# Kernel optimization log

Hardware: AMD Instinct MI355X
Metric: run time of the kernel (lower is better)

## Reference

```python
import jax, jax.numpy as jnp
import numpy as np

V, B, P = 32, 128, 256   # views/directions, batch, max points per diagram
J = 75                   # n_elements (structure elements)
NF = 32                  # n_filters (= directions)
S2 = 25                  # stage_2_out
NU = 0.1
BN_EPS = 1e-5


def _transform(births, lifetimes):
    """UpperDiagonalThresholdedLogTransform(nu=0.1) on (birth, death) points."""
    deaths = births + lifetimes + 0.01
    inv = jnp.asarray(1.0 / np.sqrt(2.0), births.dtype)
    x = (births + deaths) * inv          # rotated 1st coord
    y = (deaths - births) * inv          # rotated 2nd coord (persistence), > 0
    y = jnp.where(y <= NU, jnp.log(y / NU) * NU + NU, y)
    return jnp.stack([x, y], axis=-1)    # [V,B,P,2]


def _batchnorm(x, gamma, beta, axis):
    mean = x.mean(axis=axis, keepdims=True)
    var = x.var(axis=axis, keepdims=True)  # biased, training-mode BN
    return (x - mean) / jnp.sqrt(var + BN_EPS) * gamma + beta


def setup_inputs() -> dict:
    key = jax.random.key(0)
    ks = jax.random.split(key, 20)
    inp = {
        "births": jax.random.uniform(ks[0], (V, B, P), jnp.float32),
        "lifetimes": jax.random.uniform(ks[1], (V, B, P), jnp.float32),
        "mask": jax.random.randint(ks[2], (V, B, P), 0, 2).astype(jnp.int32),
        # SLayerPHT params (one SLayer per view)
        "centers": jax.random.uniform(ks[3], (V, J, 2), jnp.float32),
        "sharpness": 4.0 + 0.1 * jax.random.normal(ks[4], (V, J, 2), jnp.float32),
        # stage_1: Conv1d(3->NF, k=1, no bias), Conv1d(NF->8, k=1, no bias)
        "w1": 0.1 * jax.random.normal(ks[5], (V, NF, 3), jnp.float32),
        "w2": 0.1 * jax.random.normal(ks[6], (V, 8, NF), jnp.float32),
        # stage_2: Linear(J->S2), BN(S2), Linear(S2->S2)
        "l1_w": 0.1 * jax.random.normal(ks[7], (V, S2, J), jnp.float32),
        "l1_b": 0.1 * jax.random.normal(ks[8], (V, S2), jnp.float32),
        "bn1_g": jnp.ones((V, S2), jnp.float32),
        "bn1_b": jnp.zeros((V, S2), jnp.float32),
        "l2_w": 0.1 * jax.random.normal(ks[9], (V, S2, S2), jnp.float32),
        "l2_b": 0.1 * jax.random.normal(ks[10], (V, S2), jnp.float32),
        # linear_1: Linear(V*S2 -> 500) + BN(500); linear_2: Linear(500 -> 200)
        "fc1_w": 0.05 * jax.random.normal(ks[11], (500, V * S2), jnp.float32),
        "fc1_b": 0.05 * jax.random.normal(ks[12], (500,), jnp.float32),
        "bn2_g": jnp.ones((500,), jnp.float32),
        "bn2_b": jnp.zeros((500,), jnp.float32),
        "fc2_w": 0.05 * jax.random.normal(ks[13], (200, 500), jnp.float32),
        "fc2_b": 0.05 * jax.random.normal(ks[14], (200,), jnp.float32),
    }
    return inp


def reference(births, lifetimes, mask, centers, sharpness, w1, w2,
              l1_w, l1_b, bn1_g, bn1_b, l2_w, l2_b,
              fc1_w, fc1_b, bn2_g, bn2_b, fc2_w, fc2_b):
    q = _transform(births, lifetimes)                 # [V,B,P,2]
    m = mask.astype(q.dtype)                          # [V,B,P]
    # SLayer: z[v,b,j] = sum_p m * exp(-sum_d s[v,j,d]^2 (q[v,b,p,d]-c[v,j,d])^2)
    s2 = sharpness * sharpness                        # [V,J,2]
    qa = jnp.concatenate([q * q, q, jnp.ones_like(q[..., :1])], axis=-1)  # [V,B,P,5]
    ca = jnp.concatenate([s2, -2.0 * s2 * centers,
                          (s2 * centers * centers).sum(-1, keepdims=True)], axis=-1)  # [V,J,5]
    d2 = jnp.einsum('vbpk,vjk->vbpj', qa, ca)         # squared weighted distance
    z = jnp.einsum('vbpj,vbp->vbj', jnp.exp(-d2), m)  # [V,B,J]
    # neighbor-direction stacking (n_neighbor_directions=1, cyclic): [i-1, i, i+1]
    zn = jnp.stack([jnp.roll(z, 1, axis=0), z, jnp.roll(z, -1, axis=0)], axis=2)  # [V,B,3,J]
    # stage_1: two 1x1 conv1d (no bias), then max over channels
    h = jnp.einsum('vbcj,vfc->vbfj', zn, w1)          # [V,B,NF,J]
    h = jnp.einsum('vbfj,vgf->vbgj', h, w2)           # [V,B,8,J]
    h = h.max(axis=2)                                 # [V,B,J]
    # stage_2: Linear -> BN(train) -> Linear -> ReLU (Dropout = eval identity)
    u = jnp.einsum('vbj,voj->vbo', h, l1_w) + l1_b[:, None, :]   # [V,B,S2]
    u = _batchnorm(u, bn1_g[:, None, :], bn1_b[:, None, :], axis=1)
    u = jnp.einsum('vbo,vpo->vbp', u, l2_w) + l2_b[:, None, :]
    u = jax.nn.relu(u)
    x = u.transpose(1, 0, 2).reshape(B, V * S2)       # torch.cat(x, 1)
    x = x @ fc1_w.T + fc1_b
    x = _batchnorm(x, bn2_g, bn2_b, axis=0)
    x = x @ fc2_w.T + fc2_b                           # [B,200]
    return x
```

## Files before the change

kernel.cpp:

```cpp
#include <hip/hip_runtime.h>

#define V 32
#define B 128
#define P 256
#define J 75
#define NF 32
#define S2 25

__global__ __launch_bounds__(128) void slayer_kernel(
    const float* __restrict__ births,
    const float* __restrict__ lifetimes,
    const int* __restrict__ mask,
    const float* __restrict__ centers,
    const float* __restrict__ sharpness,
    float* __restrict__ z)
{
    const int vb = blockIdx.x;
    const int v  = vb >> 7;
    const int tid = threadIdx.x;
    const int lane = tid & 63;

    __shared__ float4 pts[P];
    __shared__ int cnt;

    if (tid == 0) cnt = 0;
    __syncthreads();

    const float inv = 0.70710678118654752f;
    #pragma unroll
    for (int c = 0; c < 2; ++c) {
        const int p  = tid + c * 128;
        const int gi = vb * P + p;
        float b0 = births[gi];
        float l0 = lifetimes[gi];
        int   m  = mask[gi];
        float d  = b0 + l0 + 0.01f;
        float x  = (b0 + d) * inv;
        float y  = (d - b0) * inv;
        if (y <= 0.1f) y = __logf(y * 10.0f) * 0.1f + 0.1f;

        bool keep = (m != 0);
        unsigned long long bal = __ballot(keep);
        unsigned long long lt  = (1ull << lane) - 1ull;
        int prefix = __popcll(bal & lt);
        int total  = __popcll(bal);
        int base = 0;
        if (lane == 0) base = atomicAdd(&cnt, total);
        base = __shfl(base, 0, 64);
        if (keep) pts[base + prefix] = make_float4(x, y, x * x, y * y);
    }
    __syncthreads();

    const int n = cnt;
    if (tid < J) {
        const int cj = (v * J + tid) * 2;
        float cx = centers[cj + 0];
        float cy = centers[cj + 1];
        float sx = sharpness[cj + 0];
        float sy = sharpness[cj + 1];
        float s2x = sx * sx, s2y = sy * sy;
        float k0 = -s2x;
        float k1 = -s2y;
        float k2 = 2.0f * s2x * cx;
        float k3 = 2.0f * s2y * cy;
        float kc = -(s2x * cx * cx + s2y * cy * cy);
        float acc = 0.f;
        #pragma unroll 4
        for (int p = 0; p < n; ++p) {
            float4 a = pts[p];
            float d = fmaf(k0, a.z, kc);
            d = fmaf(k1, a.w, d);
            d = fmaf(k2, a.x, d);
            d = fmaf(k3, a.y, d);
            acc += __expf(d);
        }
        z[vb * J + tid] = acc;
    }
}

__global__ __launch_bounds__(128) void stage12_kernel(
    const float* __restrict__ z,
    const float* __restrict__ w1,
    const float* __restrict__ w2,
    const float* __restrict__ l1_w,
    const float* __restrict__ l1_b,
    float* __restrict__ u_pre)
{
    const int vb = blockIdx.x;
    const int v  = vb >> 7;
    const int b  = vb & 127;
    const int vm = (v + V - 1) & (V - 1);
    const int vp = (v + 1) & (V - 1);
    const int tid = threadIdx.x;

    __shared__ float z0[J], z1[J], z2[J];
    __shared__ float w1s[NF * 3];
    __shared__ float w2s[8 * NF];
    __shared__ float hsh[J];

    if (tid < J) {
        z0[tid] = z[(vm * B + b) * J + tid];
        z1[tid] = z[(v  * B + b) * J + tid];
        z2[tid] = z[(vp * B + b) * J + tid];
    }
    if (tid < NF * 3) w1s[tid] = w1[v * NF * 3 + tid];
    w2s[tid]       = w2[v * 8 * NF + tid];
    w2s[tid + 128] = w2[v * 8 * NF + tid + 128];
    __syncthreads();

    if (tid < J) {
        float a0 = z0[tid], a1 = z1[tid], a2 = z2[tid];
        float hf[NF];
        #pragma unroll
        for (int f = 0; f < NF; ++f)
            hf[f] = w1s[f * 3 + 0] * a0 + w1s[f * 3 + 1] * a1 + w1s[f * 3 + 2] * a2;
        float hm = -3.4e38f;
        #pragma unroll
        for (int g = 0; g < 8; ++g) {
            float s = 0.f;
            #pragma unroll
            for (int f = 0; f < NF; ++f) s += w2s[g * NF + f] * hf[f];
            hm = fmaxf(hm, s);
        }
        hsh[tid] = hm;
    }
    __syncthreads();

    if (tid < S2) {
        float acc = l1_b[v * S2 + tid];
        const float* wrow = l1_w + (v * S2 + tid) * J;
        for (int j = 0; j < J; ++j) acc += hsh[j] * wrow[j];
        u_pre[vb * S2 + tid] = acc;
    }
}

__global__ __launch_bounds__(256) void bn1_l2_kernel(
    const float* __restrict__ u_pre,
    const float* __restrict__ bn1_g,
    const float* __restrict__ bn1_b,
    const float* __restrict__ l2_w,
    const float* __restrict__ l2_b,
    float* __restrict__ xT)
{
    const int v = blockIdx.x;
    const int tid = threadIdx.x;

    __shared__ float u[B * S2];
    __shared__ float w[S2 * S2];
    __shared__ float sc[S2], sh[S2];

    for (int i = tid; i < B * S2; i += 256) u[i] = u_pre[v * B * S2 + i];
    for (int i = tid; i < S2 * S2; i += 256) w[i] = l2_w[v * S2 * S2 + i];
    __syncthreads();

    if (tid < S2) {
        float s = 0.f, ss = 0.f;
        for (int b = 0; b < B; ++b) {
            float x = u[b * S2 + tid];
            s += x; ss += x * x;
        }
        float mean = s * (1.f / B);
        float var  = ss * (1.f / B) - mean * mean;
        float istd = rsqrtf(var + 1e-5f);
        float g  = bn1_g[v * S2 + tid];
        float be = bn1_b[v * S2 + tid];
        sc[tid] = g * istd;
        sh[tid] = be - mean * g * istd;
    }
    __syncthreads();

    for (int i = tid; i < B * S2; i += 256) {
        int o = i % S2;
        u[i] = u[i] * sc[o] + sh[o];
    }
    __syncthreads();

    for (int i = tid; i < B * S2; i += 256) {
        int b = i & 127;
        int p = i >> 7;
        float acc = l2_b[v * S2 + p];
        #pragma unroll
        for (int o = 0; o < S2; ++o) acc += u[b * S2 + o] * w[p * S2 + o];
        acc = fmaxf(acc, 0.f);
        xT[(v * S2 + p) * B + b] = acc;
    }
}

#define FC1_TILE 2
__global__ __launch_bounds__(128) void fc1_bn2_kernel(
    const float* __restrict__ xT,
    const float* __restrict__ fc1_w,
    const float* __restrict__ fc1_b,
    const float* __restrict__ bn2_g,
    const float* __restrict__ bn2_b,
    float* __restrict__ y1n)
{
    const int n0 = blockIdx.x * FC1_TILE;
    const int tid = threadIdx.x;
    const int K = V * S2;

    __shared__ float wsm[FC1_TILE][V * S2];
    __shared__ float red[2][2][FC1_TILE];

    for (int i = tid; i < FC1_TILE * K; i += 128) {
        int ni = i / K;
        int k  = i - ni * K;
        wsm[ni][k] = fc1_w[(n0 + ni) * K + k];
    }
    __syncthreads();

    float acc[FC1_TILE] = {0.f, 0.f};
    for (int k = 0; k < K; ++k) {
        float xv = xT[k * B + tid];
        #pragma unroll
        for (int ni = 0; ni < FC1_TILE; ++ni) acc[ni] += xv * wsm[ni][k];
    }

    const int wave = tid >> 6;
    const int lane = tid & 63;
    #pragma unroll
    for (int ni = 0; ni < FC1_TILE; ++ni) {
        acc[ni] += fc1_b[n0 + ni];
        float s = acc[ni], ss = acc[ni] * acc[ni];
        #pragma unroll
        for (int off = 32; off > 0; off >>= 1) {
            s  += __shfl_down(s,  off, 64);
            ss += __shfl_down(ss, off, 64);
        }
        if (lane == 0) { red[wave][0][ni] = s; red[wave][1][ni] = ss; }
    }
    __syncthreads();

    #pragma unroll
    for (int ni = 0; ni < FC1_TILE; ++ni) {
        float s  = red[0][0][ni] + red[1][0][ni];
        float ss = red[0][1][ni] + red[1][1][ni];
        float mean = s * (1.f / B);
        float var  = ss * (1.f / B) - mean * mean;
        float istd = rsqrtf(var + 1e-5f);
        float g  = bn2_g[n0 + ni];
        float be = bn2_b[n0 + ni];
        float scl = g * istd;
        y1n[(n0 + ni) * B + tid] = acc[ni] * scl + (be - mean * scl);
    }
}

__global__ __launch_bounds__(128) void fc2_kernel(
    const float* __restrict__ y1n,
    const float* __restrict__ fc2_w,
    const float* __restrict__ fc2_b,
    float* __restrict__ out)
{
    const int k = blockIdx.x;
    const int tid = threadIdx.x;

    __shared__ float wsm[500];
    for (int i = tid; i < 500; i += 128) wsm[i] = fc2_w[k * 500 + i];
    __syncthreads();

    float acc = fc2_b[k];
    for (int n = 0; n < 500; ++n) acc += y1n[n * B + tid] * wsm[n];
    out[tid * 200 + k] = acc;
}

extern "C" void kernel_launch(void* const* d_in, const int* in_sizes, int n_in,
                              void* d_out, int out_size, void* d_ws, size_t ws_size,
                              hipStream_t stream) {
    const float* births    = (const float*)d_in[0];
    const float* lifetimes = (const float*)d_in[1];
    const int*   mask      = (const int*)d_in[2];
    const float* centers   = (const float*)d_in[3];
    const float* sharpness = (const float*)d_in[4];
    const float* w1        = (const float*)d_in[5];
    const float* w2        = (const float*)d_in[6];
    const float* l1_w      = (const float*)d_in[7];
    const float* l1_b      = (const float*)d_in[8];
    const float* bn1_g     = (const float*)d_in[9];
    const float* bn1_b     = (const float*)d_in[10];
    const float* l2_w      = (const float*)d_in[11];
    const float* l2_b      = (const float*)d_in[12];
    const float* fc1_w     = (const float*)d_in[13];
    const float* fc1_b     = (const float*)d_in[14];
    const float* bn2_g     = (const float*)d_in[15];
    const float* bn2_b     = (const float*)d_in[16];
    const float* fc2_w     = (const float*)d_in[17];
    const float* fc2_b     = (const float*)d_in[18];
    float* out = (float*)d_out;

    float* ws    = (float*)d_ws;
    float* z     = ws;
    float* u_pre = ws + 307200;
    float* xT    = ws + 307200 + 102400;
    float* y1n   = ws + 307200 + 102400 + 102400;

    slayer_kernel <<<V * B, 128, 0, stream>>>(births, lifetimes, mask, centers, sharpness, z);
    stage12_kernel<<<V * B, 128, 0, stream>>>(z, w1, w2, l1_w, l1_b, u_pre);
    bn1_l2_kernel <<<V, 256, 0, stream>>>(u_pre, bn1_g, bn1_b, l2_w, l2_b, xT);
    fc1_bn2_kernel<<<(500 / FC1_TILE), 128, 0, stream>>>(xT, fc1_w, fc1_b, bn2_g, bn2_b, y1n);
    fc2_kernel    <<<200, 128, 0, stream>>>(y1n, fc2_w, fc2_b, out);
}
```

Before: 184.0 us.

## Split reductions across more threads in all kernels and batch stage12 per block

The SLayer kernel now uses 256 threads and splits the point loop three ways per center, combining the partial sums through shared memory. stage12 handles three batch rows per block, caches l1_w in shared memory and spreads the l1 dot products over more threads. The BN1 statistics, fc1 and fc2 split their K reductions across extra threads. The aim is to fix low thread utilisation, where only 75 or 25 threads were active, at the cost of extra syncs and shared-memory traffic.

```diff
diff --git a/kernel.cpp b/kernel.cpp
--- a/kernel.cpp
+++ b/kernel.cpp
@@ -7,7 +7,7 @@
 #define NF 32
 #define S2 25
 
-__global__ __launch_bounds__(128) void slayer_kernel(
+__global__ __launch_bounds__(256) void slayer_kernel(
     const float* __restrict__ births,
     const float* __restrict__ lifetimes,
     const int* __restrict__ mask,
@@ -22,15 +22,14 @@
 
     __shared__ float4 pts[P];
     __shared__ int cnt;
+    __shared__ float part[2][J];
 
     if (tid == 0) cnt = 0;
     __syncthreads();
 
     const float inv = 0.70710678118654752f;
-    #pragma unroll
-    for (int c = 0; c < 2; ++c) {
-        const int p  = tid + c * 128;
-        const int gi = vb * P + p;
+    {
+        const int gi = vb * P + tid;
         float b0 = births[gi];
         float l0 = lifetimes[gi];
         int   m  = mask[gi];
@@ -52,8 +51,11 @@
     __syncthreads();
 
     const int n = cnt;
-    if (tid < J) {
-        const int cj = (v * J + tid) * 2;
+    float acc = 0.f;
+    if (tid < 3 * J) {
+        const int pid = tid / J;
+        const int j   = tid - pid * J;
+        const int cj  = (v * J + j) * 2;
         float cx = centers[cj + 0];
         float cy = centers[cj + 1];
         float sx = sharpness[cj + 0];
@@ -64,9 +66,10 @@
         float k2 = 2.0f * s2x * cx;
         float k3 = 2.0f * s2y * cy;
         float kc = -(s2x * cx * cx + s2y * cy * cy);
-        float acc = 0.f;
+        const int p0 = (n * pid) / 3;
+        const int p1 = (n * (pid + 1)) / 3;
         #pragma unroll 4
-        for (int p = 0; p < n; ++p) {
+        for (int p = p0; p < p1; ++p) {
             float4 a = pts[p];
             float d = fmaf(k0, a.z, kc);
             d = fmaf(k1, a.w, d);
@@ -74,11 +77,16 @@
             d = fmaf(k3, a.y, d);
             acc += __expf(d);
         }
-        z[vb * J + tid] = acc;
-    }
-}
-
-__global__ __launch_bounds__(128) void stage12_kernel(
+        if (pid > 0) part[pid - 1][j] = acc;
+    }
+    __syncthreads();
+
+    if (tid < J)
+        z[vb * J + tid] = acc + part[0][tid] + part[1][tid];
+}
+
+#define BCH 43
+__global__ __launch_bounds__(256) void stage12_kernel(
     const float* __restrict__ z,
     const float* __restrict__ w1,
     const float* __restrict__ w2,
@@ -86,30 +94,45 @@
     const float* __restrict__ l1_b,
     float* __restrict__ u_pre)
 {
-    const int vb = blockIdx.x;
-    const int v  = vb >> 7;
-    const int b  = vb & 127;
+    const int bb    = blockIdx.x;
+    const int v     = bb / BCH;
+    const int chunk = bb - v * BCH;
+    const int b0    = chunk * 3;
+    const int nb    = (b0 + 3 <= B) ? 3 : (B - b0);
     const int vm = (v + V - 1) & (V - 1);
     const int vp = (v + 1) & (V - 1);
     const int tid = threadIdx.x;
 
-    __shared__ float z0[J], z1[J], z2[J];
     __shared__ float w1s[NF * 3];
     __shared__ float w2s[8 * NF];
-    __shared__ float hsh[J];
-
-    if (tid < J) {
-        z0[tid] = z[(vm * B + b) * J + tid];
-        z1[tid] = z[(v  * B + b) * J + tid];
-        z2[tid] = z[(vp * B + b) * J + tid];
-    }
+    __shared__ float l1ws[S2 * J];
+    __shared__ float l1bs[S2];
+    __shared__ float zsh[3][3 * J];
+    __shared__ float hshA[3 * J];
+    __shared__ float lred[3][J];
+
     if (tid < NF * 3) w1s[tid] = w1[v * NF * 3 + tid];
-    w2s[tid]       = w2[v * 8 * NF + tid];
-    w2s[tid + 128] = w2[v * 8 * NF + tid + 128];
-    __syncthreads();
-
-    if (tid < J) {
-        float a0 = z0[tid], a1 = z1[tid], a2 = z2[tid];
+    if (tid < 8 * NF) w2s[tid] = w2[v * 8 * NF + tid];
+    for (int i = tid; i < S2 * J; i += 256) l1ws[i] = l1_w[v * S2 * J + i];
+    if (tid < S2) l1bs[tid] = l1_b[v * S2 + tid];
+
+    for (int i = tid; i < nb * 3 * J; i += 256) {
+        int bl    = i / (3 * J);
+        int r     = i - bl * (3 * J);
+        int which = r / J;
+        int j     = r - which * J;
+        int b     = b0 + bl;
+        int vsrc  = (which == 0) ? vm : ((which == 1) ? v : vp);
+        zsh[bl][which * J + j] = z[(vsrc * B + b) * J + j];
+    }
+    __syncthreads();
+
+    if (tid < nb * J) {
+        int bl = tid / J;
+        int j  = tid - bl * J;
+        float a0 = zsh[bl][0 * J + j];
+        float a1 = zsh[bl][1 * J + j];
+        float a2 = zsh[bl][2 * J + j];
         float hf[NF];
         #pragma unroll
         for (int f = 0; f < NF; ++f)
@@ -122,15 +145,29 @@
             for (int f = 0; f < NF; ++f) s += w2s[g * NF + f] * hf[f];
             hm = fmaxf(hm, s);
         }
-        hsh[tid] = hm;
-    }
-    __syncthreads();
-
-    if (tid < S2) {
-        float acc = l1_b[v * S2 + tid];
-        const float* wrow = l1_w + (v * S2 + tid) * J;
-        for (int j = 0; j < J; ++j) acc += hsh[j] * wrow[j];
-        u_pre[vb * S2 + tid] = acc;
+        hshA[bl * J + j] = hm;
+    }
+    __syncthreads();
+
+    if (tid < nb * J) {
+        int bl = tid / J;
+        int r  = tid - bl * J;
+        int o  = r / 3;
+        int kk = r - o * 3;
+        const float* wrow = l1ws + o * J + kk * 25;
+        const float* hrow = hshA + bl * J + kk * 25;
+        float acc = 0.f;
+        #pragma unroll
+        for (int j = 0; j < 25; ++j) acc += hrow[j] * wrow[j];
+        lred[bl][r] = acc;
+    }
+    __syncthreads();
+
+    if (tid < nb * S2) {
+        int bl = tid / S2;
+        int o  = tid - bl * S2;
+        float acc = l1bs[o] + lred[bl][o * 3 + 0] + lred[bl][o * 3 + 1] + lred[bl][o * 3 + 2];
+        u_pre[(v * B + b0 + bl) * S2 + o] = acc;
     }
 }
 
@@ -147,18 +184,30 @@
 
     __shared__ float u[B * S2];
     __shared__ float w[S2 * S2];
+    __shared__ float sred[8 * S2], ssred[8 * S2];
     __shared__ float sc[S2], sh[S2];
 
     for (int i = tid; i < B * S2; i += 256) u[i] = u_pre[v * B * S2 + i];
     for (int i = tid; i < S2 * S2; i += 256) w[i] = l2_w[v * S2 * S2 + i];
     __syncthreads();
 
+    if (tid < 8 * S2) {
+        int c = tid / S2;
+        int o = tid - c * S2;
+        float s = 0.f, ss = 0.f;
+        #pragma unroll
+        for (int b = c * 16; b < c * 16 + 16; ++b) {
+            float x = u[b * S2 + o];
+            s += x; ss += x * x;
+        }
+        sred[tid] = s; ssred[tid] = ss;
+    }
+    __syncthreads();
+
     if (tid < S2) {
         float s = 0.f, ss = 0.f;
-        for (int b = 0; b < B; ++b) {
-            float x = u[b * S2 + tid];
-            s += x; ss += x * x;
-        }
+        #pragma unroll
+        for (int c = 0; c < 8; ++c) { s += sred[c * S2 + tid]; ss += ssred[c * S2 + tid]; }
         float mean = s * (1.f / B);
         float var  = ss * (1.f / B) - mean * mean;
         float istd = rsqrtf(var + 1e-5f);
@@ -186,8 +235,7 @@
     }
 }
 
-#define FC1_TILE 2
-__global__ __launch_bounds__(128) void fc1_bn2_kernel(
+__global__ __launch_bounds__(256) void fc1_bn2_kernel(
     const float* __restrict__ xT,
     const float* __restrict__ fc1_w,
     const float* __restrict__ fc1_b,
@@ -195,72 +243,81 @@
     const float* __restrict__ bn2_b,
     float* __restrict__ y1n)
 {
-    const int n0 = blockIdx.x * FC1_TILE;
-    const int tid = threadIdx.x;
-    const int K = V * S2;
-
-    __shared__ float wsm[FC1_TILE][V * S2];
-    __shared__ float red[2][2][FC1_TILE];
-
-    for (int i = tid; i < FC1_TILE * K; i += 128) {
-        int ni = i / K;
-        int k  = i - ni * K;
-        wsm[ni][k] = fc1_w[(n0 + ni) * K + k];
-    }
-    __syncthreads();
-
-    float acc[FC1_TILE] = {0.f, 0.f};
-    for (int k = 0; k < K; ++k) {
-        float xv = xT[k * B + tid];
-        #pragma unroll
-        for (int ni = 0; ni < FC1_TILE; ++ni) acc[ni] += xv * wsm[ni][k];
-    }
-
-    const int wave = tid >> 6;
-    const int lane = tid & 63;
-    #pragma unroll
-    for (int ni = 0; ni < FC1_TILE; ++ni) {
-        acc[ni] += fc1_b[n0 + ni];
-        float s = acc[ni], ss = acc[ni] * acc[ni];
+    const int n  = blockIdx.x;
+    const int tid = threadIdx.x;
+    const int kk = tid >> 7;
+    const int b  = tid & 127;
+    const int K  = V * S2;
+
+    __shared__ float wsm[V * S2];
+    __shared__ float pr[B];
+    __shared__ float red[2][2];
+
+    for (int i = tid; i < K; i += 256) wsm[i] = fc1_w[n * K + i];
+    __syncthreads();
+
+    float acc = 0.f;
+    const float* xp = xT + kk * 400 * B + b;
+    const float* wp = wsm + kk * 400;
+    for (int k = 0; k < 400; ++k) acc += xp[k * B] * wp[k];
+
+    if (kk == 1) pr[b] = acc;
+    __syncthreads();
+
+    float t = 0.f;
+    if (kk == 0) {
+        t = acc + pr[b] + fc1_b[n];
+        const int wave = tid >> 6;
+        const int lane = tid & 63;
+        float s = t, ss = t * t;
         #pragma unroll
         for (int off = 32; off > 0; off >>= 1) {
             s  += __shfl_down(s,  off, 64);
             ss += __shfl_down(ss, off, 64);
         }
-        if (lane == 0) { red[wave][0][ni] = s; red[wave][1][ni] = ss; }
-    }
-    __syncthreads();
-
-    #pragma unroll
-    for (int ni = 0; ni < FC1_TILE; ++ni) {
-        float s  = red[0][0][ni] + red[1][0][ni];
-        float ss = red[0][1][ni] + red[1][1][ni];
+        if (lane == 0) { red[wave][0] = s; red[wave][1] = ss; }
+    }
+    __syncthreads();
+
+    if (kk == 0) {
+        float s  = red[0][0] + red[1][0];
+        float ss = red[0][1] + red[1][1];
         float mean = s * (1.f / B);
         float var  = ss * (1.f / B) - mean * mean;
         float istd = rsqrtf(var + 1e-5f);
-        float g  = bn2_g[n0 + ni];
-        float be = bn2_b[n0 + ni];
+        float g   = bn2_g[n];
+        float be  = bn2_b[n];
         float scl = g * istd;
-        y1n[(n0 + ni) * B + tid] = acc[ni] * scl + (be - mean * scl);
-    }
-}
-
-__global__ __launch_bounds__(128) void fc2_kernel(
+        y1n[n * B + b] = t * scl + (be - mean * scl);
+    }
+}
+
+__global__ __launch_bounds__(256) void fc2_kernel(
     const float* __restrict__ y1n,
     const float* __restrict__ fc2_w,
     const float* __restrict__ fc2_b,
     float* __restrict__ out)
 {
-    const int k = blockIdx.x;
-    const int tid = threadIdx.x;
+    const int n2 = blockIdx.x;
+    const int tid = threadIdx.x;
+    const int kk = tid >> 7;
+    const int b  = tid & 127;
 
     __shared__ float wsm[500];
-    for (int i = tid; i < 500; i += 128) wsm[i] = fc2_w[k * 500 + i];
-    __syncthreads();
-
-    float acc = fc2_b[k];
-    for (int n = 0; n < 500; ++n) acc += y1n[n * B + tid] * wsm[n];
-    out[tid * 200 + k] = acc;
+    __shared__ float pr[B];
+    for (int i = tid; i < 500; i += 256) wsm[i] = fc2_w[n2 * 500 + i];
+    __syncthreads();
+
+    float acc = 0.f;
+    const float* yp = y1n + kk * 250 * B + b;
+    const float* wp = wsm + kk * 250;
+    for (int k = 0; k < 250; ++k) acc += yp[k * B] * wp[k];
+
+    if (kk == 1) pr[b] = acc;
+    __syncthreads();
+
+    if (kk == 0)
+        out[b * 200 + n2] = acc + pr[b] + fc2_b[n2];
 }
 
 extern "C" void kernel_launch(void* const* d_in, const int* in_sizes, int n_in,
@@ -293,9 +350,9 @@
     float* xT    = ws + 307200 + 102400;
     float* y1n   = ws + 307200 + 102400 + 102400;
 
-    slayer_kernel <<<V * B, 128, 0, stream>>>(births, lifetimes, mask, centers, sharpness, z);
-    stage12_kernel<<<V * B, 128, 0, stream>>>(z, w1, w2, l1_w, l1_b, u_pre);
+    slayer_kernel <<<V * B, 256, 0, stream>>>(births, lifetimes, mask, centers, sharpness, z);
+    stage12_kernel<<<V * BCH, 256, 0, stream>>>(z, w1, w2, l1_w, l1_b, u_pre);
     bn1_l2_kernel <<<V, 256, 0, stream>>>(u_pre, bn1_g, bn1_b, l2_w, l2_b, xT);
-    fc1_bn2_kernel<<<(500 / FC1_TILE), 128, 0, stream>>>(xT, fc1_w, fc1_b, bn2_g, bn2_b, y1n);
-    fc2_kernel    <<<200, 128, 0, stream>>>(y1n, fc2_w, fc2_b, out);
-}
+    fc1_bn2_kernel<<<500, 256, 0, stream>>>(xT, fc1_w, fc1_b, bn2_g, bn2_b, y1n);
+    fc2_kernel    <<<200, 256, 0, stream>>>(y1n, fc2_w, fc2_b, out);
+}
```

New measurement: 153.0 us. -16.9%, faster.
